# Kernel tuning notes

Hardware: AMD Instinct MI355X
Metric: run time of the kernel (lower is better)

## Reference

```python
import jax, jax.numpy as jnp
import numpy as np

B, O, M, H, E = 32, 64, 128, 4, 64  # batch, num_obj, memory_len, heads, embed


def setup_inputs() -> dict:
    key = jax.random.key(0)
    ks = jax.random.split(key, 10)
    s = 1.0 / np.sqrt(E)
    return {
        "query": jax.random.normal(ks[0], (B, O, E), jnp.float32),
        "context": jax.random.normal(ks[1], (B, M, E), jnp.float32),
        "memory": jax.random.normal(ks[2], (B, M, E), jnp.float32),
        "W_ch": jax.random.normal(ks[3], (E, H * E), jnp.float32) * s,
        "b_ch": jax.random.normal(ks[4], (H * E,), jnp.float32) * s,
        "w_logit": jax.random.normal(ks[5], (E,), jnp.float32) * s,
        "b_logit": jax.random.normal(ks[6], (1,), jnp.float32) * s,
        "W_rh": jax.random.normal(ks[7], (H * E, E), jnp.float32) * (1.0 / np.sqrt(H * E)),
        "b_rh": jax.random.normal(ks[8], (E,), jnp.float32) * (1.0 / np.sqrt(H * E)),
        "temp": jnp.float32(1.0),
    }


def reference(query, context, memory, W_ch, b_ch, w_logit, b_logit, W_rh, b_rh, temp):
    # create heads: [B,O,E] -> [B,O,H,E]
    q = (query @ W_ch + b_ch).reshape(B, O, H, E)
    # broadcast add query heads and context over memory axis: [B,O,M,H,E]
    qc = jnp.tanh(context[:, None, :, None, :] + q[:, :, None, :, :])
    # logit projection -> [B,O,M,H]
    logits = jnp.einsum("bomhe,e->bomh", qc, w_logit) + b_logit[0]
    # softmax over memory axis (dim=2)
    probs = jax.nn.softmax(logits / temp, axis=2)
    # weighted sum of memory over M: [B,O,H,E]
    heads = jnp.einsum("bomh,bme->bohe", probs, memory)
    heads = jax.nn.leaky_relu(heads, negative_slope=0.01)
    out = heads.reshape(B, O, H * E) @ W_rh + b_rh
    return out
```

## Files before the change

kernel.cpp:

```cpp
#include <hip/hip_runtime.h>
#include <hip/hip_fp16.h>

#define B 32
#define O 64
#define M 128
#define H 4
#define E 64
#define SC 2.88539008177792681f
#define LOG2E 1.44269504088896341f

#if __has_builtin(__builtin_amdgcn_exp2f)
#define EXP2F(x) __builtin_amdgcn_exp2f(x)
#else
#define EXP2F(x) __exp2f(x)
#endif

__device__ __forceinline__ float rl(float v, int lane) {
    return __uint_as_float(__builtin_amdgcn_readlane(__float_as_uint(v), lane));
}
__device__ __forceinline__ unsigned pk2h(float a, float b) {
    return (unsigned)__half_as_ushort(__float2half_rn(a)) |
           ((unsigned)__half_as_ushort(__float2half_rn(b)) << 16);
}

__global__ __launch_bounds__(256) void prep_kernel(
    const float* __restrict__ query, const float* __restrict__ context,
    const float* __restrict__ memory, const float* __restrict__ W_ch,
    const float* __restrict__ b_ch,
    float* __restrict__ ctx_E, __half* __restrict__ mem_h, float* __restrict__ q_E)
{
    __shared__ float s[128 * 68];
    const int t = threadIdx.x, blk = blockIdx.x;

    if (blk < 32) {
        const int b = blk;
        const float* ctx = context + b * (M * E);
        #pragma unroll
        for (int i = 0; i < 8; ++i) {
            int idx = i * 1024 + t * 4;
            float4 v = *(const float4*)(ctx + idx);
            int m = idx >> 6, e = idx & 63;
            *(float4*)(&s[m * 68 + e]) = v;
        }
        {
            const float* mem = memory + b * (M * E);
            __half* mh = mem_h + (size_t)b * (M * E);
            #pragma unroll
            for (int i = 0; i < 8; ++i) {
                int idx = i * 1024 + t * 4;
                float4 v = *(const float4*)(mem + idx);
                *(uint2*)(mh + idx) = make_uint2(pk2h(v.x, v.y), pk2h(v.z, v.w));
            }
        }
        __syncthreads();
        {
            int e = t >> 2, mb = (t & 3) * 32;
            float4* dst = (float4*)(ctx_E + (size_t)b * (E * M) + e * M + mb);
            #pragma unroll
            for (int i = 0; i < 8; ++i) {
                float4 v;
                v.x = EXP2F(SC * s[(mb + 4 * i + 0) * 68 + e]);
                v.y = EXP2F(SC * s[(mb + 4 * i + 1) * 68 + e]);
                v.z = EXP2F(SC * s[(mb + 4 * i + 2) * 68 + e]);
                v.w = EXP2F(SC * s[(mb + 4 * i + 3) * 68 + e]);
                dst[i] = v;
            }
        }
    } else {
        const int r0 = (blk - 32) * 4;
        s[t] = query[(r0 + (t & 3)) * 64 + (t >> 2)];
        __syncthreads();
        float bc = b_ch[t];
        float a0 = bc, a1 = bc, a2 = bc, a3 = bc;
        #pragma unroll 8
        for (int k = 0; k < 64; ++k) {
            float4 qv = *(const float4*)(&s[k * 4]);
            float wv = W_ch[k * 256 + t];
            a0 = fmaf(qv.x, wv, a0);
            a1 = fmaf(qv.y, wv, a1);
            a2 = fmaf(qv.z, wv, a2);
            a3 = fmaf(qv.w, wv, a3);
        }
        float* qa = q_E + (size_t)r0 * 256 + t;
        qa[0]   = EXP2F(SC * a0);
        qa[256] = EXP2F(SC * a1);
        qa[512] = EXP2F(SC * a2);
        qa[768] = EXP2F(SC * a3);
    }
}

__global__ __launch_bounds__(256) void attn_main(
    const float* __restrict__ ctx_E, const __half* __restrict__ mem_h,
    const float* __restrict__ q_E, const float* __restrict__ w_logit,
    const float* __restrict__ b_logit, const float* __restrict__ temp,
    __half* __restrict__ heads_h)
{
    __shared__ float s_E[E * M];
    __shared__ float s_prob[M * H];
    __shared__ float s_part[H * 4 * E];

    const int t = threadIdx.x, lane = t & 63, w = t >> 6;
    const int bo = blockIdx.x, b = bo >> 6;

    {
        const uint4* g1 = (const uint4*)(ctx_E + (size_t)b * (E * M));
        uint4* l1 = (uint4*)s_E;
        #pragma unroll
        for (int p = 0; p < 8; ++p)
            l1[p * 256 + t] = g1[p * 256 + t];
    }
    const float qE = q_E[bo * 256 + t];
    const float wl = w_logit[lane];
    float sumw = wl;
    #pragma unroll
    for (int sft = 1; sft < 64; sft <<= 1) sumw += __shfl_xor(sumw, sft);
    const float bl  = b_logit[0];
    const float lsc = LOG2E / temp[0];
    const float base = (sumw + bl) * lsc;
    const float lsc2 = -2.0f * lsc;
    __syncthreads();

    float acc0 = 0.f, acc1 = 0.f;
    const float2* Ep = (const float2*)s_E;
    #pragma unroll 8
    for (int e = 0; e < 64; ++e) {
        float2 Ec = Ep[e * 64 + lane];
        float Eq = rl(qE, e);
        float we = rl(wl, e);
        float a0 = fmaf(Ec.x, Eq, 1.0f);
        float a1 = fmaf(Ec.y, Eq, 1.0f);
        float r  = __builtin_amdgcn_rcpf(a0 * a1);
        acc0 = fmaf(we, a1 * r, acc0);
        acc1 = fmaf(we, a0 * r, acc1);
    }

    float l0 = fmaf(lsc2, acc0, base);
    float l1 = fmaf(lsc2, acc1, base);
    float mx = fmaxf(l0, l1);
    #pragma unroll
    for (int sft = 1; sft < 64; sft <<= 1) mx = fmaxf(mx, __shfl_xor(mx, sft));
    float e0 = EXP2F(l0 - mx);
    float e1 = EXP2F(l1 - mx);
    float sum = e0 + e1;
    #pragma unroll
    for (int sft = 1; sft < 64; sft <<= 1) sum += __shfl_xor(sum, sft);
    float rs = __builtin_amdgcn_rcpf(sum);
    s_prob[(2 * lane) * H + w]     = e0 * rs;
    s_prob[(2 * lane + 1) * H + w] = e1 * rs;
    __syncthreads();

    float h0 = 0.f, h1 = 0.f, h2 = 0.f, h3 = 0.f;
    {
        const __half* mem = mem_h + (size_t)b * (M * E) + lane;
        #pragma unroll 8
        for (int i = 0; i < 32; ++i) {
            int m = 32 * w + i;
            float4 p = *(const float4*)(&s_prob[m * 4]);
            float mv = __half2float(mem[m * 64]);
            h0 = fmaf(p.x, mv, h0);
            h1 = fmaf(p.y, mv, h1);
            h2 = fmaf(p.z, mv, h2);
            h3 = fmaf(p.w, mv, h3);
        }
    }
    s_part[0 * 256 + w * 64 + lane] = h0;
    s_part[1 * 256 + w * 64 + lane] = h1;
    s_part[2 * 256 + w * 64 + lane] = h2;
    s_part[3 * 256 + w * 64 + lane] = h3;
    __syncthreads();
    float hv = s_part[w * 256 + lane] + s_part[w * 256 + 64 + lane]
             + s_part[w * 256 + 128 + lane] + s_part[w * 256 + 192 + lane];
    hv = (hv > 0.f) ? hv : 0.01f * hv;
    heads_h[(size_t)bo * 256 + t] = __float2half_rn(hv);
}

__global__ __launch_bounds__(256) void post_kernel(
    const __half* __restrict__ heads_h, const float* __restrict__ W_rh,
    const float* __restrict__ b_rh, float* __restrict__ out)
{
    __shared__ __half s_h[4 * 256];
    const int t = threadIdx.x, lane = t & 63, r = t >> 6;
    const int r0 = blockIdx.x * 4;
    ((uint4*)s_h)[t & 127] = ((const uint4*)(heads_h + (size_t)r0 * 256))[t & 127];
    __syncthreads();
    const __half2* hr = (const __half2*)(s_h + r * 256);
    const float* Wp = W_rh + lane;
    float acc = 0.f;
    #pragma unroll 8
    for (int jp = 0; jp < 128; ++jp) {
        float2 hh = __half22float2(hr[jp]);
        acc = fmaf(hh.x, Wp[(2 * jp) * 64], acc);
        acc = fmaf(hh.y, Wp[(2 * jp + 1) * 64], acc);
    }
    out[(size_t)(r0 + r) * 64 + lane] = acc + b_rh[lane];
}

extern "C" void kernel_launch(void* const* d_in, const int* in_sizes, int n_in,
                              void* d_out, int out_size, void* d_ws, size_t ws_size,
                              hipStream_t stream) {
    const float* query   = (const float*)d_in[0];
    const float* context = (const float*)d_in[1];
    const float* memory  = (const float*)d_in[2];
    const float* W_ch    = (const float*)d_in[3];
    const float* b_ch    = (const float*)d_in[4];
    const float* w_logit = (const float*)d_in[5];
    const float* b_logit = (const float*)d_in[6];
    const float* W_rh    = (const float*)d_in[7];
    const float* b_rh    = (const float*)d_in[8];
    const float* temp    = (const float*)d_in[9];
    float* out = (float*)d_out;

    float*  ctx_E   = (float*)d_ws;
    __half* mem_h   = (__half*)(ctx_E + (size_t)B * E * M);
    float*  q_E     = (float*)(mem_h + (size_t)B * M * E);
    __half* heads_h = (__half*)(q_E + (size_t)B * O * 256);

    prep_kernel<<<544, 256, 0, stream>>>(query, context, memory, W_ch, b_ch,
                                         ctx_E, mem_h, q_E);
    attn_main<<<B * O, 256, 0, stream>>>(ctx_E, mem_h, q_E, w_logit,
                                         b_logit, temp, heads_h);
    post_kernel<<<512, 256, 0, stream>>>(heads_h, W_rh, b_rh, out);
}
```

Measured before the change: 102.0 us.

## Process two query rows per attention block with fp16 context and transposed memory

```diff
diff --git a/kernel.cpp b/kernel.cpp
--- a/kernel.cpp
+++ b/kernel.cpp
@@ -15,9 +15,6 @@
 #define EXP2F(x) __exp2f(x)
 #endif
 
-__device__ __forceinline__ float rl(float v, int lane) {
-    return __uint_as_float(__builtin_amdgcn_readlane(__float_as_uint(v), lane));
-}
 __device__ __forceinline__ unsigned pk2h(float a, float b) {
     return (unsigned)__half_as_ushort(__float2half_rn(a)) |
            ((unsigned)__half_as_ushort(__float2half_rn(b)) << 16);
@@ -27,43 +24,57 @@
     const float* __restrict__ query, const float* __restrict__ context,
     const float* __restrict__ memory, const float* __restrict__ W_ch,
     const float* __restrict__ b_ch,
-    float* __restrict__ ctx_E, __half* __restrict__ mem_h, float* __restrict__ q_E)
+    __half* __restrict__ ctx_Eh, __half* __restrict__ mem_T, float* __restrict__ q_E)
 {
     __shared__ float s[128 * 68];
     const int t = threadIdx.x, blk = blockIdx.x;
 
     if (blk < 32) {
         const int b = blk;
+        const int e = t >> 2, mb = (t & 3) * 32;
         const float* ctx = context + b * (M * E);
         #pragma unroll
         for (int i = 0; i < 8; ++i) {
             int idx = i * 1024 + t * 4;
             float4 v = *(const float4*)(ctx + idx);
-            int m = idx >> 6, e = idx & 63;
-            *(float4*)(&s[m * 68 + e]) = v;
-        }
+            *(float4*)(&s[(idx >> 6) * 68 + (idx & 63)]) = v;
+        }
+        __syncthreads();
         {
-            const float* mem = memory + b * (M * E);
-            __half* mh = mem_h + (size_t)b * (M * E);
+            uint4* dst = (uint4*)(ctx_Eh + (size_t)b * (E * M) + e * M + mb);
             #pragma unroll
-            for (int i = 0; i < 8; ++i) {
-                int idx = i * 1024 + t * 4;
-                float4 v = *(const float4*)(mem + idx);
-                *(uint2*)(mh + idx) = make_uint2(pk2h(v.x, v.y), pk2h(v.z, v.w));
+            for (int qd = 0; qd < 4; ++qd) {
+                unsigned u[4];
+                #pragma unroll
+                for (int k = 0; k < 4; ++k) {
+                    int m0 = mb + qd * 8 + 2 * k;
+                    float ea = fminf(EXP2F(SC * s[m0 * 68 + e]), 60000.f);
+                    float eb = fminf(EXP2F(SC * s[(m0 + 1) * 68 + e]), 60000.f);
+                    u[k] = pk2h(ea, eb);
+                }
+                dst[qd] = make_uint4(u[0], u[1], u[2], u[3]);
             }
         }
         __syncthreads();
+        const float* mem = memory + b * (M * E);
+        #pragma unroll
+        for (int i = 0; i < 8; ++i) {
+            int idx = i * 1024 + t * 4;
+            float4 v = *(const float4*)(mem + idx);
+            *(float4*)(&s[(idx >> 6) * 68 + (idx & 63)]) = v;
+        }
+        __syncthreads();
         {
-            int e = t >> 2, mb = (t & 3) * 32;
-            float4* dst = (float4*)(ctx_E + (size_t)b * (E * M) + e * M + mb);
+            uint4* dst = (uint4*)(mem_T + (size_t)b * (E * M) + e * M + mb);
             #pragma unroll
-            for (int i = 0; i < 8; ++i) {
-                float4 v;
-                v.x = EXP2F(SC * s[(mb + 4 * i + 0) * 68 + e]);
-                v.y = EXP2F(SC * s[(mb + 4 * i + 1) * 68 + e]);
-                v.z = EXP2F(SC * s[(mb + 4 * i + 2) * 68 + e]);
-                v.w = EXP2F(SC * s[(mb + 4 * i + 3) * 68 + e]);
-                dst[i] = v;
+            for (int qd = 0; qd < 4; ++qd) {
+                unsigned u[4];
+                #pragma unroll
+                for (int k = 0; k < 4; ++k) {
+                    int m0 = mb + qd * 8 + 2 * k;
+                    u[k] = pk2h(s[m0 * 68 + e], s[(m0 + 1) * 68 + e]);
+                }
+                dst[qd] = make_uint4(u[0], u[1], u[2], u[3]);
             }
         }
     } else {
@@ -90,88 +101,128 @@
 }
 
 __global__ __launch_bounds__(256) void attn_main(
-    const float* __restrict__ ctx_E, const __half* __restrict__ mem_h,
+    const __half* __restrict__ ctx_Eh, const __half* __restrict__ mem_T,
     const float* __restrict__ q_E, const float* __restrict__ w_logit,
     const float* __restrict__ b_logit, const float* __restrict__ temp,
     __half* __restrict__ heads_h)
 {
-    __shared__ float s_E[E * M];
-    __shared__ float s_prob[M * H];
-    __shared__ float s_part[H * 4 * E];
+    __shared__ __half s_E[E * M];
+    __shared__ float4 s_qwu[H * E];
+    __shared__ float  s_prob0[M * H];
+    __shared__ float  s_prob1[M * H];
+    __shared__ float  s_part0[H * 4 * E];
+    __shared__ float  s_part1[H * 4 * E];
 
     const int t = threadIdx.x, lane = t & 63, w = t >> 6;
-    const int bo = blockIdx.x, b = bo >> 6;
+    const int bo0 = blockIdx.x * 2, bo1 = bo0 + 1, b = bo0 >> 6;
 
     {
-        const uint4* g1 = (const uint4*)(ctx_E + (size_t)b * (E * M));
-        uint4* l1 = (uint4*)s_E;
+        const uint4* g = (const uint4*)(ctx_Eh + (size_t)b * (E * M));
+        uint4* l = (uint4*)s_E;
         #pragma unroll
-        for (int p = 0; p < 8; ++p)
-            l1[p * 256 + t] = g1[p * 256 + t];
-    }
-    const float qE = q_E[bo * 256 + t];
+        for (int p = 0; p < 4; ++p)
+            l[p * 256 + t] = g[p * 256 + t];
+    }
     const float wl = w_logit[lane];
+    s_qwu[t] = make_float4(wl, q_E[bo0 * 256 + t], q_E[bo1 * 256 + t], 0.f);
     float sumw = wl;
     #pragma unroll
     for (int sft = 1; sft < 64; sft <<= 1) sumw += __shfl_xor(sumw, sft);
-    const float bl  = b_logit[0];
-    const float lsc = LOG2E / temp[0];
+    const float bl   = b_logit[0];
+    const float lsc  = LOG2E / temp[0];
     const float base = (sumw + bl) * lsc;
     const float lsc2 = -2.0f * lsc;
     __syncthreads();
 
-    float acc0 = 0.f, acc1 = 0.f;
-    const float2* Ep = (const float2*)s_E;
-    #pragma unroll 8
+    float a00 = 0.f, a01 = 0.f, a10 = 0.f, a11 = 0.f;
+    const __half2* Ep = (const __half2*)s_E;
+    const float4*  qp = &s_qwu[w * 64];
+    #pragma unroll 4
     for (int e = 0; e < 64; ++e) {
-        float2 Ec = Ep[e * 64 + lane];
-        float Eq = rl(qE, e);
-        float we = rl(wl, e);
-        float a0 = fmaf(Ec.x, Eq, 1.0f);
-        float a1 = fmaf(Ec.y, Eq, 1.0f);
-        float r  = __builtin_amdgcn_rcpf(a0 * a1);
-        acc0 = fmaf(we, a1 * r, acc0);
-        acc1 = fmaf(we, a0 * r, acc1);
-    }
-
-    float l0 = fmaf(lsc2, acc0, base);
-    float l1 = fmaf(lsc2, acc1, base);
-    float mx = fmaxf(l0, l1);
+        float2 cf = __half22float2(Ep[e * 64 + lane]);
+        float4 qw = qp[e];
+        float t00 = fmaf(cf.x, qw.y, 1.0f);
+        float t01 = fmaf(cf.y, qw.y, 1.0f);
+        float t10 = fmaf(cf.x, qw.z, 1.0f);
+        float t11 = fmaf(cf.y, qw.z, 1.0f);
+        float r0 = __builtin_amdgcn_rcpf(t00 * t01);
+        float r1 = __builtin_amdgcn_rcpf(t10 * t11);
+        float w0 = qw.x * r0;
+        float w1 = qw.x * r1;
+        a00 = fmaf(w0, t01, a00);  a01 = fmaf(w0, t00, a01);
+        a10 = fmaf(w1, t11, a10);  a11 = fmaf(w1, t10, a11);
+    }
+
+    uint4 mr[4];
+    {
+        const uint4* mp = (const uint4*)(mem_T + (size_t)b * (E * M) + lane * M + 32 * w);
+        mr[0] = mp[0]; mr[1] = mp[1]; mr[2] = mp[2]; mr[3] = mp[3];
+    }
+
+    float l00 = fmaf(lsc2, a00, base), l01 = fmaf(lsc2, a01, base);
+    float l10 = fmaf(lsc2, a10, base), l11 = fmaf(lsc2, a11, base);
+    float mx0 = fmaxf(l00, l01), mx1 = fmaxf(l10, l11);
     #pragma unroll
-    for (int sft = 1; sft < 64; sft <<= 1) mx = fmaxf(mx, __shfl_xor(mx, sft));
-    float e0 = EXP2F(l0 - mx);
-    float e1 = EXP2F(l1 - mx);
-    float sum = e0 + e1;
+    for (int sft = 1; sft < 64; sft <<= 1) {
+        mx0 = fmaxf(mx0, __shfl_xor(mx0, sft));
+        mx1 = fmaxf(mx1, __shfl_xor(mx1, sft));
+    }
+    float e00 = EXP2F(l00 - mx0), e01 = EXP2F(l01 - mx0);
+    float e10 = EXP2F(l10 - mx1), e11 = EXP2F(l11 - mx1);
+    float s0 = e00 + e01, s1 = e10 + e11;
     #pragma unroll
-    for (int sft = 1; sft < 64; sft <<= 1) sum += __shfl_xor(sum, sft);
-    float rs = __builtin_amdgcn_rcpf(sum);
-    s_prob[(2 * lane) * H + w]     = e0 * rs;
-    s_prob[(2 * lane + 1) * H + w] = e1 * rs;
-    __syncthreads();
-
-    float h0 = 0.f, h1 = 0.f, h2 = 0.f, h3 = 0.f;
+    for (int sft = 1; sft < 64; sft <<= 1) {
+        s0 += __shfl_xor(s0, sft);
+        s1 += __shfl_xor(s1, sft);
+    }
+    float rs0 = __builtin_amdgcn_rcpf(s0), rs1 = __builtin_amdgcn_rcpf(s1);
+    s_prob0[(2 * lane) * H + w]     = e00 * rs0;
+    s_prob0[(2 * lane + 1) * H + w] = e01 * rs0;
+    s_prob1[(2 * lane) * H + w]     = e10 * rs1;
+    s_prob1[(2 * lane + 1) * H + w] = e11 * rs1;
+    __syncthreads();
+
+    float h00 = 0.f, h01 = 0.f, h02 = 0.f, h03 = 0.f;
+    float h10 = 0.f, h11 = 0.f, h12 = 0.f, h13 = 0.f;
     {
-        const __half* mem = mem_h + (size_t)b * (M * E) + lane;
+        union { uint4 u4[4]; __half2 h2[16]; } mu;
+        mu.u4[0] = mr[0]; mu.u4[1] = mr[1]; mu.u4[2] = mr[2]; mu.u4[3] = mr[3];
+        const int mbase = 32 * w;
         #pragma unroll 8
-        for (int i = 0; i < 32; ++i) {
-            int m = 32 * w + i;
-            float4 p = *(const float4*)(&s_prob[m * 4]);
-            float mv = __half2float(mem[m * 64]);
-            h0 = fmaf(p.x, mv, h0);
-            h1 = fmaf(p.y, mv, h1);
-            h2 = fmaf(p.z, mv, h2);
-            h3 = fmaf(p.w, mv, h3);
-        }
-    }
-    s_part[0 * 256 + w * 64 + lane] = h0;
-    s_part[1 * 256 + w * 64 + lane] = h1;
-    s_part[2 * 256 + w * 64 + lane] = h2;
-    s_part[3 * 256 + w * 64 + lane] = h3;
-    __syncthreads();
-    float hv = s_part[w * 256 + lane] + s_part[w * 256 + 64 + lane]
-             + s_part[w * 256 + 128 + lane] + s_part[w * 256 + 192 + lane];
-    hv = (hv > 0.f) ? hv : 0.01f * hv;
-    heads_h[(size_t)bo * 256 + t] = __float2half_rn(hv);
+        for (int j = 0; j < 16; ++j) {
+            float2 mv = __half22float2(mu.h2[j]);
+            int m = mbase + 2 * j;
+            float4 pa = *(const float4*)(&s_prob0[m * 4]);
+            float4 pb = *(const float4*)(&s_prob0[(m + 1) * 4]);
+            h00 = fmaf(pa.x, mv.x, h00); h01 = fmaf(pa.y, mv.x, h01);
+            h02 = fmaf(pa.z, mv.x, h02); h03 = fmaf(pa.w, mv.x, h03);
+            h00 = fmaf(pb.x, mv.y, h00); h01 = fmaf(pb.y, mv.y, h01);
+            h02 = fmaf(pb.z, mv.y, h02); h03 = fmaf(pb.w, mv.y, h03);
+            float4 pc = *(const float4*)(&s_prob1[m * 4]);
+            float4 pd = *(const float4*)(&s_prob1[(m + 1) * 4]);
+            h10 = fmaf(pc.x, mv.x, h10); h11 = fmaf(pc.y, mv.x, h11);
+            h12 = fmaf(pc.z, mv.x, h12); h13 = fmaf(pc.w, mv.x, h13);
+            h10 = fmaf(pd.x, mv.y, h10); h11 = fmaf(pd.y, mv.y, h11);
+            h12 = fmaf(pd.z, mv.y, h12); h13 = fmaf(pd.w, mv.y, h13);
+        }
+    }
+    s_part0[0 * 256 + w * 64 + lane] = h00;
+    s_part0[1 * 256 + w * 64 + lane] = h01;
+    s_part0[2 * 256 + w * 64 + lane] = h02;
+    s_part0[3 * 256 + w * 64 + lane] = h03;
+    s_part1[0 * 256 + w * 64 + lane] = h10;
+    s_part1[1 * 256 + w * 64 + lane] = h11;
+    s_part1[2 * 256 + w * 64 + lane] = h12;
+    s_part1[3 * 256 + w * 64 + lane] = h13;
+    __syncthreads();
+    float hv0 = s_part0[w * 256 + lane] + s_part0[w * 256 + 64 + lane]
+              + s_part0[w * 256 + 128 + lane] + s_part0[w * 256 + 192 + lane];
+    float hv1 = s_part1[w * 256 + lane] + s_part1[w * 256 + 64 + lane]
+              + s_part1[w * 256 + 128 + lane] + s_part1[w * 256 + 192 + lane];
+    hv0 = (hv0 > 0.f) ? hv0 : 0.01f * hv0;
+    hv1 = (hv1 > 0.f) ? hv1 : 0.01f * hv1;
+    heads_h[(size_t)bo0 * 256 + t] = __float2half_rn(hv0);
+    heads_h[(size_t)bo1 * 256 + t] = __float2half_rn(hv1);
 }
 
 __global__ __launch_bounds__(256) void post_kernel(
@@ -210,14 +261,14 @@
     const float* temp    = (const float*)d_in[9];
     float* out = (float*)d_out;
 
-    float*  ctx_E   = (float*)d_ws;
-    __half* mem_h   = (__half*)(ctx_E + (size_t)B * E * M);
-    float*  q_E     = (float*)(mem_h + (size_t)B * M * E);
+    __half* ctx_Eh  = (__half*)d_ws;
+    __half* mem_T   = ctx_Eh + (size_t)B * E * M;
+    float*  q_E     = (float*)(mem_T + (size_t)B * E * M);
     __half* heads_h = (__half*)(q_E + (size_t)B * O * 256);
 
     prep_kernel<<<544, 256, 0, stream>>>(query, context, memory, W_ch, b_ch,
-                                         ctx_E, mem_h, q_E);
-    attn_main<<<B * O, 256, 0, stream>>>(ctx_E, mem_h, q_E, w_logit,
-                                         b_logit, temp, heads_h);
+                                         ctx_Eh, mem_T, q_E);
+    attn_main<<<B * O / 2, 256, 0, stream>>>(ctx_Eh, mem_T, q_E, w_logit,
+                                             b_logit, temp, heads_h);
     post_kernel<<<512, 256, 0, stream>>>(heads_h, W_rh, b_rh, out);
 }
```

Result: no change. 101.8 us (-0.2%).
